# Performance work log

Measured on AMD Instinct MI355X. Metric: run time of the kernel, lower is better.

## Reference

```python
import jax, jax.numpy as jnp
import numpy as np

B, T, I = 32, 128, 512
H, L, O = 512, 2, 512


def _uniform(key, shape, std):
    return jax.random.uniform(key, shape, jnp.float32, -std, std)


def setup_inputs() -> dict:
    key = jax.random.key(0)
    ks = jax.random.split(key, 12)
    std = 1.0 / np.sqrt(H)
    inp = {
        "x": jax.random.normal(ks[0], (B, T, I), jnp.float32),
        # stacked params: [L, 2, ...]; dir 0 = forward cells, dir 1 = reverse cells
        "Wxh": _uniform(ks[1], (L, 2, I, 2 * H), std),
        "bxh": _uniform(ks[2], (L, 2, 2 * H), std),
        "Whh": _uniform(ks[3], (L, 2, H, 2 * H), std),
        "bhh": _uniform(ks[4], (L, 2, 2 * H), std),
        "Wxr": _uniform(ks[5], (L, 2, I, H), std),
        "bxr": _uniform(ks[6], (L, 2, H), std),
        "Whr": _uniform(ks[7], (L, 2, H, H), std),
        "bhr": _uniform(ks[8], (L, 2, H, ), std),
        "Wfc": _uniform(ks[9], (2 * H, O), 1.0 / np.sqrt(2 * H)),
        "bfc": _uniform(ks[10], (O,), 1.0 / np.sqrt(2 * H)),
    }
    return inp


def gru_layer(seq, Wxh_l, bxh_l, Whh_l, bhh_l, Wxr_l, bxr_l, Whr_l, bhr_l):
    # seq: [T, B, I]. Precompute input projections for all timesteps (one big GEMM),
    # then scan the sequential h-dependent part.
    xh = jnp.einsum('tbi,ih->tbh', seq, Wxh_l) + bxh_l  # [T,B,2H]
    xr = jnp.einsum('tbi,ih->tbh', seq, Wxr_l) + bxr_l  # [T,B,H]

    def step(h, inp):
        xh_t, xr_t = inp
        zr = xh_t + h @ Whh_l + bhh_l
        z, r = jnp.split(zr, 2, axis=-1)
        z = jax.nn.sigmoid(z)
        r = jax.nn.sigmoid(r)
        g = jnp.tanh((h @ Whr_l + bhr_l) * r + xr_t)
        h = z * h + (1.0 - z) * g
        return h, h

    h0 = jnp.zeros((seq.shape[1], Whh_l.shape[0]), seq.dtype)
    _, out = jax.lax.scan(step, h0, (xh, xr))
    return out  # [T,B,H]


def reference(x, Wxh, bxh, Whh, bhh, Wxr, bxr, Whr, bhr, Wfc, bfc):
    # Faithful translation of BidirRecurrentModel.forward (GRU mode):
    # forward stream scans time-ordered input; reverse stream independently scans
    # the time-reversed input (the two streams are NOT concatenated between layers).
    seq_f = jnp.transpose(x, (1, 0, 2))   # [T,B,I]
    seq_r = seq_f[::-1]                   # reversed time order
    n_layers = Wxh.shape[0]
    for l in range(n_layers):
        seq_f = gru_layer(seq_f, Wxh[l, 0], bxh[l, 0], Whh[l, 0], bhh[l, 0],
                          Wxr[l, 0], bxr[l, 0], Whr[l, 0], bhr[l, 0])
        seq_r = gru_layer(seq_r, Wxh[l, 1], bxh[l, 1], Whh[l, 1], bhh[l, 1],
                          Wxr[l, 1], bxr[l, 1], Whr[l, 1], bhr[l, 1])
    # out = last fwd timestep; out_rev = FIRST element of reverse-ordered stream
    # (i.e. the reverse cell's state after one step), exactly as in the source.
    out = jnp.concatenate([seq_f[-1], seq_r[0]], axis=1)  # [B, 2H]
    return out @ Wfc + bfc  # [B, O]
```

## Files before the change

kernel.cpp:

```cpp
#include <hip/hip_runtime.h>
#include <hip/hip_bf16.h>

#define PROJ_ELEMS 12582912
#define SEQ_ELEMS  4194304
#define SLAB_PER_BLK 6144

typedef float f32x4 __attribute__((ext_vector_type(4)));

__device__ unsigned g_slots[512];

__global__ __launch_bounds__(256)
void proj_kernel(const float* __restrict__ src,
                 const float* __restrict__ Wxh, const float* __restrict__ bxh,
                 const float* __restrict__ Wxr, const float* __restrict__ bxr,
                 __hip_bfloat16* __restrict__ proj, int layer)
{
    __shared__ float As[32][137];
    __shared__ float Ws[32][132];
    const int tid  = threadIdx.x;
    const int col0 = blockIdx.x * 128;
    const int row0 = blockIdx.y * 128;
    const int d    = row0 >> 12;
    const int ld   = layer * 2 + d;
    const int tx = tid & 15, ty = tid >> 4;

    const bool is_xr = (col0 >= 1024);
    const float* Wbase = is_xr ? (Wxr + (size_t)ld * 512 * 512 + (col0 - 1024))
                               : (Wxh + (size_t)ld * 512 * 1024 + col0);
    const int wstride = is_xr ? 512 : 1024;
    const float* bias = is_xr ? (bxr + ld * 512 + (col0 - 1024))
                              : (bxh + ld * 1024 + col0);

    float acc[8][8];
    #pragma unroll
    for (int i = 0; i < 8; i++)
        #pragma unroll
        for (int j = 0; j < 8; j++) acc[i][j] = 0.f;

    for (int k0 = 0; k0 < 512; k0 += 32) {
        #pragma unroll
        for (int v = 0; v < 4; v++) {
            int idx = tid + v * 256;
            int r   = idx >> 3;
            int c4  = (idx & 7) << 2;
            int gm  = row0 + r;
            int rr  = gm & 4095;
            int tt  = rr >> 5, bb = rr & 31;
            const float* p;
            if (layer == 0) {
                int ts = (gm >= 4096) ? (127 - tt) : tt;
                p = src + ((size_t)bb * 128 + ts) * 512 + (k0 + c4);
            } else {
                p = src + (((size_t)(gm >> 12) * 128 + tt) * 32 + bb) * 512 + (k0 + c4);
            }
            float4 vv = *(const float4*)p;
            As[c4 + 0][r] = vv.x; As[c4 + 1][r] = vv.y;
            As[c4 + 2][r] = vv.z; As[c4 + 3][r] = vv.w;
        }
        #pragma unroll
        for (int v = 0; v < 4; v++) {
            int idx = tid + v * 256;
            int kr  = idx >> 5;
            int c4  = (idx & 31) << 2;
            *(float4*)&Ws[kr][c4] = *(const float4*)(Wbase + (size_t)(k0 + kr) * wstride + c4);
        }
        __syncthreads();
        #pragma unroll
        for (int kk = 0; kk < 32; kk++) {
            float a[8], w[8];
            *(float4*)&a[0] = *(const float4*)&As[kk][ty * 8];
            *(float4*)&a[4] = *(const float4*)&As[kk][ty * 8 + 4];
            *(float4*)&w[0] = *(const float4*)&Ws[kk][tx * 8];
            *(float4*)&w[4] = *(const float4*)&Ws[kk][tx * 8 + 4];
            #pragma unroll
            for (int i = 0; i < 8; i++)
                #pragma unroll
                for (int j = 0; j < 8; j++)
                    acc[i][j] += a[i] * w[j];
        }
        __syncthreads();
    }
    #pragma unroll
    for (int i = 0; i < 8; i++) {
        int gm = row0 + ty * 8 + i;
        __hip_bfloat16* dst = proj + (size_t)gm * 1536 + col0 + tx * 8;
        #pragma unroll
        for (int j = 0; j < 8; j++)
            dst[j] = __float2bfloat16(acc[i][j] + bias[tx * 8 + j]);
    }
}

__global__ __launch_bounds__(256)
void repack_kernel(const float* __restrict__ Whh, const float* __restrict__ Whr,
                   float* __restrict__ slabs)
{
    if (blockIdx.x == 0) {
        g_slots[threadIdx.x] = 0u;
        g_slots[threadIdx.x + 256] = 0u;
    }
    const int blk = blockIdx.x;
    const int ld = blk >> 7, jb = blk & 127;
    const float* WhhL = Whh + (size_t)ld * 512 * 1024;
    const float* WhrL = Whr + (size_t)ld * 512 * 512;
    float* out = slabs + (size_t)blk * SLAB_PER_BLK;
    for (int u = 0; u < 24; u++) {
        int idx = threadIdx.x + u * 256;
        int rec = idx / 12, r3 = idx % 12;
        int g = rec >> 2, cg = rec & 3;
        int e = r3 >> 2, ki = r3 & 3;
        int k = g * 4 + ki, j = jb * 4 + cg;
        float v;
        if (e == 0)      v = WhhL[(size_t)k * 1024 + j];
        else if (e == 1) v = WhhL[(size_t)k * 1024 + 512 + j];
        else             v = WhrL[(size_t)k * 512 + j];
        out[idx] = v;
    }
}

__global__ __launch_bounds__(1024, 4)
void gru_seq_kernel(const __hip_bfloat16* __restrict__ proj, float* __restrict__ seq,
                    const float* __restrict__ slabs,
                    const float* __restrict__ bhh, const float* __restrict__ bhr,
                    int layer)
{
    __shared__ __align__(16) float wlds[4100];
    const int tid = threadIdx.x;
    const int d   = blockIdx.x >> 7;
    const int jb  = blockIdx.x & 127;
    const int ld  = layer * 2 + d;
    const int cgi = tid & 3;
    const int kq  = (tid >> 2) & 7;
    const int b   = tid >> 5;
    const int j   = jb * 4 + cgi;

    const f32x4* wrec = (const f32x4*)slabs + (size_t)(ld * 128 + jb) * 1536;
    const float bz = bhh[ld * 1024 + j];
    const float br = bhh[ld * 1024 + 512 + j];
    const float bg = bhr[ld * 512 + j];
    const float* hbase = seq + (size_t)(d * 128) * 32 * 512;
    const __hip_bfloat16* pbase = proj + ((size_t)(d * 128) * 32 + b) * 1536 + j;
    float* wout = seq + ((size_t)(d * 128) * 32 + b) * 512 + j;
    unsigned* slot_base = &g_slots[ld * 128];
    unsigned* s0p = slot_base + (tid & 63);
    unsigned* s1p = s0p + 64;

    {
        int i = tid;
        ((f32x4*)wlds)[i + (i >= 512 ? 1 : 0)] = wrec[(i >> 1) * 3 + (i & 1)];
    }

    __hip_bfloat16 rz = pbase[0], rr_ = pbase[512], rg = pbase[1024];
    float hv_prev = 0.f;

    for (int t = 0; t < 128; ++t) {
        float az = 0.f, ar = 0.f, ag = 0.f;
        if (t > 0) {
            const unsigned tgt = (unsigned)t;
            for (;;) {
                unsigned a = __hip_atomic_load(s0p, __ATOMIC_RELAXED,
                                               __HIP_MEMORY_SCOPE_AGENT);
                unsigned c = __hip_atomic_load(s1p, __ATOMIC_RELAXED,
                                               __HIP_MEMORY_SCOPE_AGENT);
                if (__all(a >= tgt && c >= tgt)) break;
                __builtin_amdgcn_s_sleep(1);
            }
            asm volatile("" ::: "memory");

            const float* hrow = hbase + (size_t)(t - 1) * 32 * 512 + b * 512;
            #pragma unroll 8
            for (int gg = 0; gg < 16; gg++) {
                int g   = kq * 16 + gg;
                int rec = g * 4 + cgi;
                float4 h4 = *(const float4*)(hrow + g * 4);
                const f32x4* wp = (const f32x4*)wlds + (rec << 1) + (kq >> 2);
                f32x4 wz = wp[0], wr = wp[1];
                f32x4 wg = wrec[rec * 3 + 2];
                az += h4.x * wz.x + h4.y * wz.y + h4.z * wz.z + h4.w * wz.w;
                ar += h4.x * wr.x + h4.y * wr.y + h4.z * wr.z + h4.w * wr.w;
                ag += h4.x * wg.x + h4.y * wg.y + h4.z * wg.z + h4.w * wg.w;
            }
            az += __shfl_xor(az, 4, 64);  ar += __shfl_xor(ar, 4, 64);  ag += __shfl_xor(ag, 4, 64);
            az += __shfl_xor(az, 8, 64);  ar += __shfl_xor(ar, 8, 64);  ag += __shfl_xor(ag, 8, 64);
            az += __shfl_xor(az, 16, 64); ar += __shfl_xor(ar, 16, 64); ag += __shfl_xor(ag, 16, 64);
        }

        float pz = __bfloat162float(rz);
        float pr = __bfloat162float(rr_);
        float pg = __bfloat162float(rg);
        float z  = 1.f / (1.f + __expf(-(az + pz + bz)));
        float r  = 1.f / (1.f + __expf(-(ar + pr + br)));
        float gt = tanhf((ag + bg) * r + pg);
        float hn = z * hv_prev + (1.f - z) * gt;
        hv_prev = hn;
        if (kq == 0)
            __hip_atomic_store(wout + (size_t)t * 32 * 512, hn,
                               __ATOMIC_RELAXED, __HIP_MEMORY_SCOPE_AGENT);

        if (t < 127) {
            __syncthreads();
            if (tid == 0)
                __hip_atomic_store(slot_base + jb, (unsigned)(t + 1),
                                   __ATOMIC_RELAXED, __HIP_MEMORY_SCOPE_AGENT);
            const __hip_bfloat16* pn = pbase + (size_t)(t + 1) * 32 * 1536;
            rz = pn[0]; rr_ = pn[512]; rg = pn[1024];
        }
    }
}

__global__ __launch_bounds__(256)
void fc_kernel(const float* __restrict__ seq, const float* __restrict__ Wfc,
               const float* __restrict__ bfc, float* __restrict__ out)
{
    int idx = blockIdx.x * 256 + threadIdx.x;
    int b = idx >> 9, o = idx & 511;
    const float* catf = seq + ((size_t)(0 * 128 + 127) * 32 + b) * 512;
    const float* catr = seq + ((size_t)(1 * 128 + 0) * 32 + b) * 512;
    float acc = bfc[o];
    #pragma unroll 8
    for (int k = 0; k < 512; k++) acc += catf[k] * Wfc[(size_t)k * 512 + o];
    #pragma unroll 8
    for (int k = 0; k < 512; k++) acc += catr[k] * Wfc[(size_t)(512 + k) * 512 + o];
    out[(size_t)b * 512 + o] = acc;
}

extern "C" void kernel_launch(void* const* d_in, const int* in_sizes, int n_in,
                              void* d_out, int out_size, void* d_ws, size_t ws_size,
                              hipStream_t stream) {
    (void)in_sizes; (void)n_in; (void)out_size; (void)ws_size;
    const float* x   = (const float*)d_in[0];
    const float* Wxh = (const float*)d_in[1];
    const float* bxh = (const float*)d_in[2];
    const float* Whh = (const float*)d_in[3];
    const float* bhh = (const float*)d_in[4];
    const float* Wxr = (const float*)d_in[5];
    const float* bxr = (const float*)d_in[6];
    const float* Whr = (const float*)d_in[7];
    const float* bhr = (const float*)d_in[8];
    const float* Wfc = (const float*)d_in[9];
    const float* bfc = (const float*)d_in[10];
    float* out = (float*)d_out;

    char* base = (char*)d_ws;
    __hip_bfloat16* proj = (__hip_bfloat16*)base;
    float* seq   = (float*)(base + (size_t)PROJ_ELEMS * 2);
    float* slabs = seq + SEQ_ELEMS;

    repack_kernel<<<512, 256, 0, stream>>>(Whh, Whr, slabs);

    dim3 pgrid(12, 64);
    proj_kernel<<<pgrid, 256, 0, stream>>>(x, Wxh, bxh, Wxr, bxr, proj, 0);
    {
        int layer = 0;
        void* args[] = {(void*)&proj, (void*)&seq, (void*)&slabs,
                        (void*)&bhh, (void*)&bhr, (void*)&layer};
        hipLaunchCooperativeKernel((void*)gru_seq_kernel, dim3(256), dim3(1024),
                                   args, 0, stream);
    }
    proj_kernel<<<pgrid, 256, 0, stream>>>(seq, Wxh, bxh, Wxr, bxr, proj, 1);
    {
        int layer = 1;
        void* args[] = {(void*)&proj, (void*)&seq, (void*)&slabs,
                        (void*)&bhh, (void*)&bhr, (void*)&layer};
        hipLaunchCooperativeKernel((void*)gru_seq_kernel, dim3(256), dim3(1024),
                                   args, 0, stream);
    }
    fc_kernel<<<64, 256, 0, stream>>>(seq, Wfc, bfc, out);
}
```

Measured before the change: 3.104 ms.

## Replace block-wide barrier with per-wavefront flags and stage h through LDS

Each wavefront now publishes and polls its own progress flag, with one flag set per wave and direction, so the per-step __syncthreads and the single-thread flag store go away. Every wave loads its two batch rows of the previous hidden state once, using cache-bypassing loads, into a swizzled LDS buffer and reads them back from there, where before each thread read its slice straight from global memory. The spin-wait backs off to a longer sleep after a few polls. In exchange the kernel uses more LDS and more flag memory, and correctness now depends on the hand-written vmcnt waits and the per-wave ordering of stores.

```diff
diff --git a/kernel.cpp b/kernel.cpp
--- a/kernel.cpp
+++ b/kernel.cpp
@@ -7,7 +7,7 @@
 
 typedef float f32x4 __attribute__((ext_vector_type(4)));
 
-__device__ unsigned g_slots[512];
+__device__ unsigned g_slots[8192];
 
 __global__ __launch_bounds__(256)
 void proj_kernel(const float* __restrict__ src,
@@ -94,10 +94,8 @@
 void repack_kernel(const float* __restrict__ Whh, const float* __restrict__ Whr,
                    float* __restrict__ slabs)
 {
-    if (blockIdx.x == 0) {
-        g_slots[threadIdx.x] = 0u;
-        g_slots[threadIdx.x + 256] = 0u;
-    }
+    if (blockIdx.x == 0)
+        for (int i = threadIdx.x; i < 8192; i += 256) g_slots[i] = 0u;
     const int blk = blockIdx.x;
     const int ld = blk >> 7, jb = blk & 127;
     const float* WhhL = Whh + (size_t)ld * 512 * 1024;
@@ -123,15 +121,19 @@
                     const float* __restrict__ bhh, const float* __restrict__ bhr,
                     int layer)
 {
+    __shared__ __align__(16) float hs[16 * 1024];
     __shared__ __align__(16) float wlds[4100];
-    const int tid = threadIdx.x;
-    const int d   = blockIdx.x >> 7;
-    const int jb  = blockIdx.x & 127;
-    const int ld  = layer * 2 + d;
-    const int cgi = tid & 3;
-    const int kq  = (tid >> 2) & 7;
-    const int b   = tid >> 5;
-    const int j   = jb * 4 + cgi;
+    const int tid  = threadIdx.x;
+    const int d    = blockIdx.x >> 7;
+    const int jb   = blockIdx.x & 127;
+    const int ld   = layer * 2 + d;
+    const int cgi  = tid & 3;
+    const int kq   = (tid >> 2) & 7;
+    const int b    = tid >> 5;
+    const int w    = tid >> 6;
+    const int lane = tid & 63;
+    const int brl  = (tid >> 5) & 1;
+    const int j    = jb * 4 + cgi;
 
     const f32x4* wrec = (const f32x4*)slabs + (size_t)(ld * 128 + jb) * 1536;
     const float bz = bhh[ld * 1024 + j];
@@ -140,14 +142,18 @@
     const float* hbase = seq + (size_t)(d * 128) * 32 * 512;
     const __hip_bfloat16* pbase = proj + ((size_t)(d * 128) * 32 + b) * 1536 + j;
     float* wout = seq + ((size_t)(d * 128) * 32 + b) * 512 + j;
-    unsigned* slot_base = &g_slots[ld * 128];
-    unsigned* s0p = slot_base + (tid & 63);
-    unsigned* s1p = s0p + 64;
+
+    unsigned* sp   = g_slots + layer * 4096 + ((w * 2 + d) << 7);
+    unsigned* s0p  = sp + lane;
+    unsigned* s1p  = sp + 64 + lane;
+    unsigned* spub = sp + jb;
+    float* hw = &hs[w * 1024];
 
     {
         int i = tid;
         ((f32x4*)wlds)[i + (i >= 512 ? 1 : 0)] = wrec[(i >> 1) * 3 + (i & 1)];
     }
+    __syncthreads();
 
     __hip_bfloat16 rz = pbase[0], rr_ = pbase[512], rg = pbase[1024];
     float hv_prev = 0.f;
@@ -156,22 +162,42 @@
         float az = 0.f, ar = 0.f, ag = 0.f;
         if (t > 0) {
             const unsigned tgt = (unsigned)t;
+            int spins = 0;
             for (;;) {
                 unsigned a = __hip_atomic_load(s0p, __ATOMIC_RELAXED,
                                                __HIP_MEMORY_SCOPE_AGENT);
                 unsigned c = __hip_atomic_load(s1p, __ATOMIC_RELAXED,
                                                __HIP_MEMORY_SCOPE_AGENT);
                 if (__all(a >= tgt && c >= tgt)) break;
-                __builtin_amdgcn_s_sleep(1);
+                if (spins < 2) { __builtin_amdgcn_s_sleep(1); spins++; }
+                else           { __builtin_amdgcn_s_sleep(8); }
             }
             asm volatile("" ::: "memory");
 
-            const float* hrow = hbase + (size_t)(t - 1) * 32 * 512 + b * 512;
+            const float* hsrc = hbase + ((size_t)(t - 1) * 32 + 2 * w) * 512;
+            f32x4 tmp[4];
+            #pragma unroll
+            for (int v = 0; v < 4; v++) {
+                int id = lane + v * 64;
+                asm volatile("global_load_dwordx4 %0, %1, off sc0 sc1"
+                             : "=v"(tmp[v])
+                             : "v"((const void*)(hsrc + (size_t)id * 4)));
+            }
+            asm volatile("s_waitcnt vmcnt(0)" ::: "memory");
+            #pragma unroll
+            for (int v = 0; v < 4; v++) {
+                int id  = lane + v * 64;
+                int row = id >> 7, g = id & 127;
+                int sl  = g ^ ((g >> 4) & 7);
+                *(f32x4*)&hw[row * 512 + (sl << 2)] = tmp[v];
+            }
+
             #pragma unroll 8
             for (int gg = 0; gg < 16; gg++) {
                 int g   = kq * 16 + gg;
+                int sl  = g ^ kq;
                 int rec = g * 4 + cgi;
-                float4 h4 = *(const float4*)(hrow + g * 4);
+                float4 h4 = *(const float4*)&hw[brl * 512 + (sl << 2)];
                 const f32x4* wp = (const f32x4*)wlds + (rec << 1) + (kq >> 2);
                 f32x4 wz = wp[0], wr = wp[1];
                 f32x4 wg = wrec[rec * 3 + 2];
@@ -197,9 +223,9 @@
                                __ATOMIC_RELAXED, __HIP_MEMORY_SCOPE_AGENT);
 
         if (t < 127) {
-            __syncthreads();
-            if (tid == 0)
-                __hip_atomic_store(slot_base + jb, (unsigned)(t + 1),
+            asm volatile("s_waitcnt vmcnt(0)" ::: "memory");
+            if (lane == 0)
+                __hip_atomic_store(spub, (unsigned)(t + 1),
                                    __ATOMIC_RELAXED, __HIP_MEMORY_SCOPE_AGENT);
             const __hip_bfloat16* pn = pbase + (size_t)(t + 1) * 32 * 1536;
             rz = pn[0]; rr_ = pn[512]; rg = pn[1024];
```

After: 7.035 ms. +126.7%, slower.
